# Kernel optimization log

Measured on AMD Instinct MI355X. Metric: run time of the kernel, lower is better.

Reference implementation:

```python
import jax, jax.numpy as jnp
import numpy as np

ITERS = 3
EPS = 1e-6


def setup_inputs() -> dict:
    key = jax.random.key(0)
    k1, k2 = jax.random.split(key, 2)
    a = jax.random.normal(k1, (64, 1152, 1, 1, 1, 1), dtype=jnp.float32)
    v = jax.random.normal(k2, (64, 1152, 32, 4, 4, 1), dtype=jnp.float32)
    logits = jnp.ones((1, 1152, 32, 1, 1, 1), dtype=jnp.float32)
    return {"a": a, "v": v, "logits": logits}


def _squash(s):
    # s: (batch, 1, B, P, P, 1); norm over dim 2 (matches torch code, dim=2)
    norm_sq = jnp.sum(s * s, axis=2, keepdims=True)
    return jnp.sqrt(norm_sq + EPS) / (1.0 + norm_sq) * s


def reference(a, v, logits):
    # a: (batch, A, 1, 1, 1, 1) -- unused (overwritten in original forward)
    # v: (batch, A, B, P, P, 1); logits: (1, A, B, 1, 1, 1)
    batch = v.shape[0]
    b = jnp.broadcast_to(logits, (batch,) + logits.shape[1:])
    p = None
    for i in range(ITERS):
        c = jax.nn.softmax(b, axis=2)                    # route over B
        s = jnp.sum(c * v, axis=1, keepdims=True)        # (batch,1,B,P,P,1)
        p = _squash(s)
        if i < ITERS - 1:
            # agreement: sum over pose dims -> (batch, A, B, 1, 1, 1)
            b = b + jnp.sum(p * v, axis=(-3, -2, -1), keepdims=True)
    p = jnp.squeeze(p, axis=1)                           # (batch, B, P, P, 1)
    a_out = jnp.linalg.norm(p, ord=2, axis=2)            # (batch, B, P, 1)
    return (a_out, p)
```

## Files before the change

kernel.cpp:

```cpp
#include <hip/hip_runtime.h>
#include <math.h>

#define BATCH 64
#define ADIM  1152
#define BDIM  32
#define POSE  16
#define SLICE 512
#define CHUNKS 16
#define WAVES 4
#define ROWS_PER_WAVE 18
#define G 3
#define NGROUPS 6
#define EPSQ 1e-6f
#define SPART_ITER ((size_t)BATCH * CHUNKS * SLICE)

template<int ITER>
__global__ __launch_bounds__(256) void route_pass(
    const float* __restrict__ v,
    const float* __restrict__ logits,
    const float* __restrict__ p_buf,
    float* __restrict__ s_out)
{
    const int bt    = blockIdx.x / CHUNKS;
    const int chunk = blockIdx.x % CHUNKS;
    const int t     = threadIdx.x;
    const int wv    = t >> 6;
    const int lane  = t & 63;
    const int bq    = lane >> 2;

    const int row0 = (chunk * WAVES + wv) * ROWS_PER_WAVE;

    float4 psA = make_float4(0.f, 0.f, 0.f, 0.f);
    float4 psB = make_float4(0.f, 0.f, 0.f, 0.f);
    if (ITER >= 1) {
        const float4* pp = (const float4*)(p_buf + (size_t)bt * SLICE);
        psA = pp[lane];
        psB = pp[64 + lane];
    }
    if (ITER >= 2) {
        const float4* pp = (const float4*)(p_buf + (size_t)(BATCH + bt) * SLICE);
        float4 a = pp[lane], b = pp[64 + lane];
        psA.x += a.x; psA.y += a.y; psA.z += a.z; psA.w += a.w;
        psB.x += b.x; psB.y += b.y; psB.z += b.z; psB.w += b.w;
    }

    float lg[9];
    {
        const float* lbase = logits + row0 * BDIM;
#pragma unroll
        for (int i = 0; i < 9; ++i) lg[i] = lbase[i * 64 + lane];
    }

    float4 acc0 = make_float4(0.f, 0.f, 0.f, 0.f);
    float4 acc1 = make_float4(0.f, 0.f, 0.f, 0.f);

    const float4* vb4 = (const float4*)(v + ((size_t)bt * ADIM + row0) * SLICE);

    float4 bufA[G][2], bufB[G][2];

    auto load_group = [&](float4 (*buf)[2], int g) {
#pragma unroll
        for (int r = 0; r < G; ++r) {
            buf[r][0] = vb4[(g * G + r) * 128 + lane];
            buf[r][1] = vb4[(g * G + r) * 128 + 64 + lane];
        }
    };

    auto compute_group = [&](float4 (*buf)[2], int g) {
#pragma unroll
        for (int r = 0; r < G; ++r) {
            const int ar = g * G + r;
            float4 va = buf[r][0];
            float4 vb = buf[r][1];

            const int base0 = ar * 32;
            const int base1 = ar * 32 + 16;
            float b0 = __shfl(lg[base0 >> 6], (base0 & 63) + bq, 64);
            float b1 = __shfl(lg[base1 >> 6], (base1 & 63) + bq, 64);

            if (ITER >= 1) {
                float d0 = psA.x * va.x + psA.y * va.y + psA.z * va.z + psA.w * va.w;
                float d1 = psB.x * vb.x + psB.y * vb.y + psB.z * vb.z + psB.w * vb.w;
                d0 += __shfl_xor(d0, 1, 64); d0 += __shfl_xor(d0, 2, 64);
                d1 += __shfl_xor(d1, 1, 64); d1 += __shfl_xor(d1, 2, 64);
                b0 += d0; b1 += d1;
            }

            float e0 = __expf(b0);
            float e1 = __expf(b1);
            float u = e0 + e1;
#pragma unroll
            for (int off = 4; off <= 32; off <<= 1)
                u += __shfl_xor(u, off, 64);
            float rd = __builtin_amdgcn_rcpf(u);
            float c0 = e0 * rd;
            float c1 = e1 * rd;

            acc0.x = fmaf(c0, va.x, acc0.x); acc0.y = fmaf(c0, va.y, acc0.y);
            acc0.z = fmaf(c0, va.z, acc0.z); acc0.w = fmaf(c0, va.w, acc0.w);
            acc1.x = fmaf(c1, vb.x, acc1.x); acc1.y = fmaf(c1, vb.y, acc1.y);
            acc1.z = fmaf(c1, vb.z, acc1.z); acc1.w = fmaf(c1, vb.w, acc1.w);
        }
    };

    load_group(bufA, 0);
#pragma unroll
    for (int g = 0; g < NGROUPS; ++g) {
        float4 (*cur)[2] = (g & 1) ? bufB : bufA;
        float4 (*nxt)[2] = (g & 1) ? bufA : bufB;
        if (g + 1 < NGROUPS) load_group(nxt, g + 1);
        compute_group(cur, g);
    }

    __shared__ float4 red[WAVES * 128];
    red[wv * 128 + lane] = acc0;
    red[wv * 128 + 64 + lane] = acc1;
    __syncthreads();

    if (t < 128) {
        float4 s = red[t];
#pragma unroll
        for (int w = 1; w < WAVES; ++w) {
            float4 x = red[w * 128 + t];
            s.x += x.x; s.y += x.y; s.z += x.z; s.w += x.w;
        }
        ((float4*)(s_out + ((size_t)bt * CHUNKS + chunk) * SLICE))[t] = s;
    }
}

__global__ __launch_bounds__(512) void squash_pass(
    const float* __restrict__ s_part_j,
    float* __restrict__ p_out_j)
{
    const int bt = blockIdx.x;
    const int t  = threadIdx.x;

    __shared__ float sq[SLICE];
    __shared__ float fac[POSE];

    float sv = 0.f;
#pragma unroll
    for (int c = 0; c < CHUNKS; ++c)
        sv += s_part_j[((size_t)bt * CHUNKS + c) * SLICE + t];

    sq[t] = sv * sv;
    __syncthreads();
    if (t < POSE) {
        float n = 0.f;
        for (int b2 = 0; b2 < BDIM; ++b2) n += sq[b2 * POSE + t];
        fac[t] = sqrtf(n + EPSQ) / (1.f + n);
    }
    __syncthreads();
    p_out_j[(size_t)bt * SLICE + t] = fac[t & 15] * sv;
}

__global__ __launch_bounds__(512) void final_out(
    const float* __restrict__ s_part2,
    float* __restrict__ out)
{
    const int bt = blockIdx.x;
    const int t  = threadIdx.x;
    const int pose = t & 15;

    __shared__ float sq[SLICE];
    __shared__ float ns[POSE];

    float sv = 0.f;
#pragma unroll
    for (int c = 0; c < CHUNKS; ++c)
        sv += s_part2[((size_t)bt * CHUNKS + c) * SLICE + t];

    sq[t] = sv * sv;
    __syncthreads();
    if (t < POSE) {
        float a = 0.f;
        for (int b2 = 0; b2 < BDIM; ++b2) a += sq[b2 * POSE + t];
        ns[t] = a;
    }
    __syncthreads();
    float n = ns[pose];
    float pv = sqrtf(n + EPSQ) / (1.f + n) * sv;

    out[8192 + bt * SLICE + t] = pv;
    sq[t] = pv * pv;
    __syncthreads();
    if (t < 128) {
        int b2 = t >> 2, p2 = t & 3;
        float a = 0.f;
#pragma unroll
        for (int p1 = 0; p1 < 4; ++p1) a += sq[b2 * POSE + p1 * 4 + p2];
        out[bt * 128 + b2 * 4 + p2] = sqrtf(a);
    }
}

extern "C" void kernel_launch(void* const* d_in, const int* in_sizes, int n_in,
                              void* d_out, int out_size, void* d_ws, size_t ws_size,
                              hipStream_t stream) {
    const float* v      = (const float*)d_in[1];
    const float* logits = (const float*)d_in[2];
    float* out = (float*)d_out;

    float* s_part = (float*)d_ws;
    float* p_buf  = s_part + 3 * SPART_ITER;

    route_pass<0><<<dim3(BATCH * CHUNKS), dim3(256), 0, stream>>>(
        v, logits, p_buf, s_part + 0 * SPART_ITER);
    squash_pass<<<dim3(BATCH), dim3(512), 0, stream>>>(
        s_part + 0 * SPART_ITER, p_buf);
    route_pass<1><<<dim3(BATCH * CHUNKS), dim3(256), 0, stream>>>(
        v, logits, p_buf, s_part + 1 * SPART_ITER);
    squash_pass<<<dim3(BATCH), dim3(512), 0, stream>>>(
        s_part + 1 * SPART_ITER, p_buf + (size_t)BATCH * SLICE);
    route_pass<2><<<dim3(BATCH * CHUNKS), dim3(256), 0, stream>>>(
        v, logits, p_buf, s_part + 2 * SPART_ITER);
    final_out<<<dim3(BATCH), dim3(512), 0, stream>>>(
        s_part + 2 * SPART_ITER, out);
}
```

Baseline: 269.6 us.

## Cache v as bf16 tile in first pass and read it in later routing passes

The first routing pass now computes the softmax of the logits once per row in shared memory, uses nontemporal loads to stream v, and writes a bf16-compressed copy of v to workspace. The two later passes read this half-size copy instead of the fp32 input, cutting their global memory traffic roughly in half. The squash pass keeps a running sum of p so the next pass reads one buffer. The cost is an extra write of the compressed tile in pass one and bf16 rounding of v in the agreement and weighted sums, which may shift the output against tolerance.

```diff
diff --git a/kernel.cpp b/kernel.cpp
--- a/kernel.cpp
+++ b/kernel.cpp
@@ -7,130 +7,165 @@
 #define POSE  16
 #define SLICE 512
 #define CHUNKS 16
+#define ROWS  72
+#define RPW   18
 #define WAVES 4
-#define ROWS_PER_WAVE 18
-#define G 3
-#define NGROUPS 6
-#define EPSQ 1e-6f
+#define EPSQ  1e-6f
 #define SPART_ITER ((size_t)BATCH * CHUNKS * SLICE)
 
-template<int ITER>
-__global__ __launch_bounds__(256) void route_pass(
+typedef float v4f __attribute__((ext_vector_type(4)));
+
+__device__ __forceinline__ unsigned pack_bf16x2(float a, float b) {
+    unsigned ua = __float_as_uint(a), ub = __float_as_uint(b);
+    ua = (ua + 0x7fffu + ((ua >> 16) & 1u)) >> 16;
+    ub = (ub + 0x7fffu + ((ub >> 16) & 1u));
+    return (ua & 0xffffu) | (ub & 0xffff0000u);
+}
+
+__device__ __forceinline__ v4f unpack_bf16x4(uint2 w) {
+    v4f r;
+    r.x = __uint_as_float(w.x << 16);
+    r.y = __uint_as_float(w.x & 0xffff0000u);
+    r.z = __uint_as_float(w.y << 16);
+    r.w = __uint_as_float(w.y & 0xffff0000u);
+    return r;
+}
+
+__global__ __launch_bounds__(256) void route0_compress(
     const float* __restrict__ v,
     const float* __restrict__ logits,
-    const float* __restrict__ p_buf,
+    uint2* __restrict__ tile,
+    float* __restrict__ s_part)
+{
+    const int bt    = blockIdx.x >> 4;
+    const int chunk = blockIdx.x & 15;
+    const int t     = threadIdx.x;
+    const int bc0   = (t >> 2) & 31;
+    const int hi    = t >> 7;
+    const int a0    = chunk * ROWS;
+
+    __shared__ float w_sh[ROWS * BDIM];
+    __shared__ v4f   red[128];
+
+    if (t < ROWS) {
+        const float* lr = logits + (size_t)(a0 + t) * BDIM;
+        float s = 0.f;
+        float e[BDIM];
+#pragma unroll
+        for (int b = 0; b < BDIM; ++b) { e[b] = __expf(lr[b]); s += e[b]; }
+        float rd = 1.f / s;
+#pragma unroll
+        for (int b = 0; b < BDIM; ++b) w_sh[t * BDIM + b] = e[b] * rd;
+    }
+    __syncthreads();
+
+    const v4f* vg = (const v4f*)(v + ((size_t)bt * ADIM + a0) * SLICE);
+    uint2*     tg = tile + ((size_t)bt * ADIM + a0) * 128;
+
+    v4f acc = (v4f){0.f, 0.f, 0.f, 0.f};
+    v4f fA[6], fB[6];
+#pragma unroll
+    for (int u = 0; u < 6; ++u)
+        fA[u] = __builtin_nontemporal_load(&vg[t + 256 * u]);
+
+#pragma unroll
+    for (int kk = 0; kk < 6; ++kk) {
+        v4f* cur = (kk & 1) ? fB : fA;
+        v4f* nxt = (kk & 1) ? fA : fB;
+        if (kk + 1 < 6) {
+#pragma unroll
+            for (int u = 0; u < 6; ++u)
+                nxt[u] = __builtin_nontemporal_load(&vg[t + 256 * ((kk + 1) * 6 + u)]);
+        }
+#pragma unroll
+        for (int u = 0; u < 6; ++u) {
+            const int k   = kk * 6 + u;
+            const int i   = t + 256 * k;
+            const int row = 2 * k + hi;
+            tg[i] = make_uint2(pack_bf16x2(cur[u].x, cur[u].y),
+                               pack_bf16x2(cur[u].z, cur[u].w));
+            float c0 = w_sh[row * BDIM + bc0];
+            acc += c0 * cur[u];
+        }
+    }
+
+    __syncthreads();
+    if (t >= 128) red[t - 128] = acc;
+    __syncthreads();
+    if (t < 128) {
+        acc += red[t];
+        ((v4f*)(s_part + ((size_t)bt * CHUNKS + chunk) * SLICE))[t] = acc;
+    }
+}
+
+__global__ __launch_bounds__(256) void route_next(
+    const uint2* __restrict__ tile,
+    const float* __restrict__ logits,
+    const float* __restrict__ psum_g,
     float* __restrict__ s_out)
 {
-    const int bt    = blockIdx.x / CHUNKS;
-    const int chunk = blockIdx.x % CHUNKS;
+    const int bt    = blockIdx.x >> 4;
+    const int chunk = blockIdx.x & 15;
     const int t     = threadIdx.x;
+    const int lane  = t & 63;
     const int wv    = t >> 6;
-    const int lane  = t & 63;
     const int bq    = lane >> 2;
-
-    const int row0 = (chunk * WAVES + wv) * ROWS_PER_WAVE;
-
-    float4 psA = make_float4(0.f, 0.f, 0.f, 0.f);
-    float4 psB = make_float4(0.f, 0.f, 0.f, 0.f);
-    if (ITER >= 1) {
-        const float4* pp = (const float4*)(p_buf + (size_t)bt * SLICE);
-        psA = pp[lane];
-        psB = pp[64 + lane];
-    }
-    if (ITER >= 2) {
-        const float4* pp = (const float4*)(p_buf + (size_t)(BATCH + bt) * SLICE);
-        float4 a = pp[lane], b = pp[64 + lane];
-        psA.x += a.x; psA.y += a.y; psA.z += a.z; psA.w += a.w;
-        psB.x += b.x; psB.y += b.y; psB.z += b.z; psB.w += b.w;
-    }
-
-    float lg[9];
-    {
-        const float* lbase = logits + row0 * BDIM;
-#pragma unroll
-        for (int i = 0; i < 9; ++i) lg[i] = lbase[i * 64 + lane];
-    }
-
-    float4 acc0 = make_float4(0.f, 0.f, 0.f, 0.f);
-    float4 acc1 = make_float4(0.f, 0.f, 0.f, 0.f);
-
-    const float4* vb4 = (const float4*)(v + ((size_t)bt * ADIM + row0) * SLICE);
-
-    float4 bufA[G][2], bufB[G][2];
-
-    auto load_group = [&](float4 (*buf)[2], int g) {
-#pragma unroll
-        for (int r = 0; r < G; ++r) {
-            buf[r][0] = vb4[(g * G + r) * 128 + lane];
-            buf[r][1] = vb4[(g * G + r) * 128 + 64 + lane];
-        }
-    };
-
-    auto compute_group = [&](float4 (*buf)[2], int g) {
-#pragma unroll
-        for (int r = 0; r < G; ++r) {
-            const int ar = g * G + r;
-            float4 va = buf[r][0];
-            float4 vb = buf[r][1];
-
-            const int base0 = ar * 32;
-            const int base1 = ar * 32 + 16;
-            float b0 = __shfl(lg[base0 >> 6], (base0 & 63) + bq, 64);
-            float b1 = __shfl(lg[base1 >> 6], (base1 & 63) + bq, 64);
-
-            if (ITER >= 1) {
-                float d0 = psA.x * va.x + psA.y * va.y + psA.z * va.z + psA.w * va.w;
-                float d1 = psB.x * vb.x + psB.y * vb.y + psB.z * vb.z + psB.w * vb.w;
-                d0 += __shfl_xor(d0, 1, 64); d0 += __shfl_xor(d0, 2, 64);
-                d1 += __shfl_xor(d1, 1, 64); d1 += __shfl_xor(d1, 2, 64);
-                b0 += d0; b1 += d1;
-            }
-
-            float e0 = __expf(b0);
-            float e1 = __expf(b1);
-            float u = e0 + e1;
-#pragma unroll
-            for (int off = 4; off <= 32; off <<= 1)
-                u += __shfl_xor(u, off, 64);
-            float rd = __builtin_amdgcn_rcpf(u);
-            float c0 = e0 * rd;
-            float c1 = e1 * rd;
-
-            acc0.x = fmaf(c0, va.x, acc0.x); acc0.y = fmaf(c0, va.y, acc0.y);
-            acc0.z = fmaf(c0, va.z, acc0.z); acc0.w = fmaf(c0, va.w, acc0.w);
-            acc1.x = fmaf(c1, vb.x, acc1.x); acc1.y = fmaf(c1, vb.y, acc1.y);
-            acc1.z = fmaf(c1, vb.z, acc1.z); acc1.w = fmaf(c1, vb.w, acc1.w);
-        }
-    };
-
-    load_group(bufA, 0);
-#pragma unroll
-    for (int g = 0; g < NGROUPS; ++g) {
-        float4 (*cur)[2] = (g & 1) ? bufB : bufA;
-        float4 (*nxt)[2] = (g & 1) ? bufA : bufB;
-        if (g + 1 < NGROUPS) load_group(nxt, g + 1);
-        compute_group(cur, g);
-    }
-
-    __shared__ float4 red[WAVES * 128];
-    red[wv * 128 + lane] = acc0;
-    red[wv * 128 + 64 + lane] = acc1;
-    __syncthreads();
-
-    if (t < 128) {
-        float4 s = red[t];
-#pragma unroll
-        for (int w = 1; w < WAVES; ++w) {
-            float4 x = red[w * 128 + t];
-            s.x += x.x; s.y += x.y; s.z += x.z; s.w += x.w;
-        }
-        ((float4*)(s_out + ((size_t)bt * CHUNKS + chunk) * SLICE))[t] = s;
+    const int a0    = chunk * ROWS;
+
+    __shared__ v4f red[WAVES * 128];
+
+    const v4f* pp = (const v4f*)(psum_g + (size_t)bt * SLICE);
+    v4f psA = pp[lane];
+    v4f psB = pp[64 + lane];
+    v4f acc0 = (v4f){0.f, 0.f, 0.f, 0.f};
+    v4f acc1 = (v4f){0.f, 0.f, 0.f, 0.f};
+
+    const int r0 = wv * RPW;
+    const uint2* tb = tile + ((size_t)bt * ADIM + a0) * 128;
+
+#pragma unroll 6
+    for (int r = 0; r < RPW; ++r) {
+        const int rw = r0 + r;
+        uint2 wa = tb[rw * 128 + lane];
+        uint2 wb = tb[rw * 128 + 64 + lane];
+        v4f va = unpack_bf16x4(wa);
+        v4f vb = unpack_bf16x4(wb);
+        float b0 = logits[(size_t)(a0 + rw) * BDIM + bq];
+        float b1 = logits[(size_t)(a0 + rw) * BDIM + 16 + bq];
+        float d0 = psA.x * va.x + psA.y * va.y + psA.z * va.z + psA.w * va.w;
+        float d1 = psB.x * vb.x + psB.y * vb.y + psB.z * vb.z + psB.w * vb.w;
+        d0 += __shfl_xor(d0, 1, 64); d0 += __shfl_xor(d0, 2, 64);
+        d1 += __shfl_xor(d1, 1, 64); d1 += __shfl_xor(d1, 2, 64);
+        float e0 = __expf(b0 + d0);
+        float e1 = __expf(b1 + d1);
+        float uu = e0 + e1;
+#pragma unroll
+        for (int off = 4; off <= 32; off <<= 1)
+            uu += __shfl_xor(uu, off, 64);
+        float rd = __builtin_amdgcn_rcpf(uu);
+        float c0 = e0 * rd, c1 = e1 * rd;
+        acc0 += c0 * va;
+        acc1 += c1 * vb;
+    }
+
+    __syncthreads();
+    if (wv == 3) { red[lane] = acc0; red[64 + lane] = acc1; }
+    __syncthreads();
+    if (wv == 2) { red[lane] += acc0; red[64 + lane] += acc1; }
+    __syncthreads();
+    if (wv == 1) { red[lane] += acc0; red[64 + lane] += acc1; }
+    __syncthreads();
+    if (wv == 0) {
+        v4f* sp = (v4f*)(s_out + ((size_t)bt * CHUNKS + chunk) * SLICE);
+        sp[lane]      = red[lane] + acc0;
+        sp[64 + lane] = red[64 + lane] + acc1;
     }
 }
 
 __global__ __launch_bounds__(512) void squash_pass(
     const float* __restrict__ s_part_j,
-    float* __restrict__ p_out_j)
+    float* __restrict__ psum,
+    int add)
 {
     const int bt = blockIdx.x;
     const int t  = threadIdx.x;
@@ -151,7 +186,8 @@
         fac[t] = sqrtf(n + EPSQ) / (1.f + n);
     }
     __syncthreads();
-    p_out_j[(size_t)bt * SLICE + t] = fac[t & 15] * sv;
+    float prev = add ? psum[(size_t)bt * SLICE + t] : 0.f;
+    psum[(size_t)bt * SLICE + t] = prev + fac[t & 15] * sv;
 }
 
 __global__ __launch_bounds__(512) void final_out(
@@ -181,15 +217,15 @@
     float n = ns[pose];
     float pv = sqrtf(n + EPSQ) / (1.f + n) * sv;
 
-    out[8192 + bt * SLICE + t] = pv;
+    out[8192 + (size_t)bt * SLICE + t] = pv;
     sq[t] = pv * pv;
     __syncthreads();
     if (t < 128) {
-        int b2 = t >> 2, p2 = t & 3;
+        const int b2 = t >> 2, p2 = t & 3;
         float a = 0.f;
 #pragma unroll
         for (int p1 = 0; p1 < 4; ++p1) a += sq[b2 * POSE + p1 * 4 + p2];
-        out[bt * 128 + b2 * 4 + p2] = sqrtf(a);
+        out[(size_t)bt * 128 + t] = sqrtf(a);
     }
 }
 
@@ -200,19 +236,20 @@
     const float* logits = (const float*)d_in[2];
     float* out = (float*)d_out;
 
-    float* s_part = (float*)d_ws;
-    float* p_buf  = s_part + 3 * SPART_ITER;
-
-    route_pass<0><<<dim3(BATCH * CHUNKS), dim3(256), 0, stream>>>(
-        v, logits, p_buf, s_part + 0 * SPART_ITER);
+    uint2* tile   = (uint2*)d_ws;
+    float* s_part = (float*)((char*)d_ws + (size_t)BATCH * ADIM * 128 * sizeof(uint2));
+    float* psum   = s_part + 3 * SPART_ITER;
+
+    route0_compress<<<dim3(BATCH * CHUNKS), dim3(256), 0, stream>>>(
+        v, logits, tile, s_part + 0 * SPART_ITER);
     squash_pass<<<dim3(BATCH), dim3(512), 0, stream>>>(
-        s_part + 0 * SPART_ITER, p_buf);
-    route_pass<1><<<dim3(BATCH * CHUNKS), dim3(256), 0, stream>>>(
-        v, logits, p_buf, s_part + 1 * SPART_ITER);
+        s_part + 0 * SPART_ITER, psum, 0);
+    route_next<<<dim3(BATCH * CHUNKS), dim3(256), 0, stream>>>(
+        tile, logits, psum, s_part + 1 * SPART_ITER);
     squash_pass<<<dim3(BATCH), dim3(512), 0, stream>>>(
-        s_part + 1 * SPART_ITER, p_buf + (size_t)BATCH * SLICE);
-    route_pass<2><<<dim3(BATCH * CHUNKS), dim3(256), 0, stream>>>(
-        v, logits, p_buf, s_part + 2 * SPART_ITER);
+        s_part + 1 * SPART_ITER, psum, 1);
+    route_next<<<dim3(BATCH * CHUNKS), dim3(256), 0, stream>>>(
+        tile, logits, psum, s_part + 2 * SPART_ITER);
     final_out<<<dim3(BATCH), dim3(512), 0, stream>>>(
         s_part + 2 * SPART_ITER, out);
 }
```

New measurement: 257.9 us. -4.4%, faster.
